# Performance work log

Hardware: AMD Instinct MI355X
Metric: run time of the kernel (lower is better)

Reference implementation:

```python
import jax, jax.numpy as jnp
import numpy as np

N = 100000   # nodes
E = 1600000  # edges
IN = 128     # in_dim
H = 64       # hidden_dim
EPS = 1e-5


def layer_norm(x, g, b):
    mu = x.mean(-1, keepdims=True)
    v = ((x - mu) ** 2).mean(-1, keepdims=True)
    return (x - mu) * jax.lax.rsqrt(v + EPS) * g + b


def gcn_conv(x, W, b, src, dst, dinv):
    # PyG GCNConv: x' = D^{-1/2}(A+I)D^{-1/2} X W + b (degrees include self-loops)
    h = x @ W                                   # [N, H]
    coef = dinv[src] * dinv[dst]                # [E]
    agg = jax.ops.segment_sum(h[src] * coef[:, None], dst, num_segments=N)
    agg = agg + h * (dinv * dinv)[:, None]      # self-loop term
    return agg + b


def setup_inputs() -> dict:
    key = jax.random.key(0)
    ks = jax.random.split(key, 12)
    inp = {
        "x": jax.random.normal(ks[0], (N, IN), jnp.float32),
        "edge_index": jax.random.randint(ks[1], (2, E), 0, N, dtype=jnp.int64
                                         if jax.config.jax_enable_x64 else jnp.int32),
    }
    dims = [(IN, H), (H, H), (H, H)]
    for i, (di, do) in enumerate(dims, start=1):
        inp[f"W{i}"] = jax.random.normal(ks[2 * i], (di, do), jnp.float32) / np.sqrt(di)
        inp[f"b{i}"] = jnp.zeros((do,), jnp.float32)
        inp[f"g{i}"] = jnp.ones((do,), jnp.float32)
        inp[f"be{i}"] = jnp.zeros((do,), jnp.float32)
    inp["Wh"] = jax.random.normal(ks[11], (H, 1), jnp.float32) / np.sqrt(H)
    inp["bh"] = jnp.zeros((1,), jnp.float32)
    return inp


def reference(x, edge_index, W1, b1, g1, be1, W2, b2, g2, be2, W3, b3, g3, be3, Wh, bh):
    src, dst = edge_index[0], edge_index[1]
    deg = jax.ops.segment_sum(jnp.ones((E,), x.dtype), dst, num_segments=N) + 1.0
    dinv = jax.lax.rsqrt(deg)
    for W, b, g, be in ((W1, b1, g1, be1), (W2, b2, g2, be2), (W3, b3, g3, be3)):
        x = gcn_conv(x, W, b, src, dst, dinv)
        x = layer_norm(x, g, be)
        x = jax.nn.gelu(x, approximate=False)  # F.gelu default = exact erf
        # dropout omitted (eval mode / deterministic reference)
    return (x @ Wh + bh).squeeze(-1)  # [N]
```

## Files before the change

### kernel.cpp

```cpp
#include <hip/hip_runtime.h>
#include <math.h>

#define NODES 100000
#define EDGES 1600000
#define SCAN_CHUNK 1024
#define NBUCK 196
#define BCAP2 12288
#define EPB 4096

typedef __attribute__((ext_vector_type(8))) short short8;
typedef __attribute__((ext_vector_type(4))) float floatx4;

__device__ __forceinline__ float half_sum(float x) {
#pragma unroll
  for (int o = 16; o > 0; o >>= 1) x += __shfl_xor(x, o, 64);
  return x;
}

__device__ __forceinline__ short f2bf(float f) {
  union { float f; unsigned u; } v;
  v.f = f;
  unsigned r = 0x7fffu + ((v.u >> 16) & 1u);
  return (short)((v.u + r) >> 16);
}
__device__ __forceinline__ float bf2f(short s) {
  union { unsigned u; float f; } v;
  v.u = ((unsigned)(unsigned short)s) << 16;
  return v.f;
}
__device__ __forceinline__ float bflo(unsigned p) {
  union { unsigned u; float f; } v; v.u = p << 16; return v.f;
}
__device__ __forceinline__ float bfhi(unsigned p) {
  union { unsigned u; float f; } v; v.u = p & 0xffff0000u; return v.f;
}

__global__ __launch_bounds__(256) void k_bin2(const int* __restrict__ src,
                                              const int* __restrict__ dst,
                                              int* __restrict__ bins,
                                              int* __restrict__ gcur) {
  __shared__ int cnt[NBUCK], gbase[NBUCK], lcur[NBUCK];
  int t = threadIdx.x;
  for (int i = t; i < NBUCK; i += 256) cnt[i] = 0;
  __syncthreads();
  int base = blockIdx.x * EPB;
  int s[16], d[16];
#pragma unroll
  for (int j = 0; j < 16; ++j) {
    int e = base + j * 256 + t;
    if (e < EDGES) {
      s[j] = src[e];
      d[j] = dst[e];
      atomicAdd(&cnt[d[j] >> 9], 1);
    } else {
      d[j] = -1;
    }
  }
  __syncthreads();
  for (int i = t; i < NBUCK; i += 256) {
    int c = cnt[i];
    gbase[i] = c ? atomicAdd(&gcur[i], c) : 0;
    lcur[i] = 0;
  }
  __syncthreads();
#pragma unroll
  for (int j = 0; j < 16; ++j) {
    if (d[j] >= 0) {
      int bk = d[j] >> 9;
      int lp = atomicAdd(&lcur[bk], 1);
      int pos = gbase[bk] + lp;
      if (pos < BCAP2) bins[bk * BCAP2 + pos] = s[j] | ((d[j] & 511) << 17);
    }
  }
}

__global__ __launch_bounds__(256) void k_hist(const int* __restrict__ bins,
                                              const int* __restrict__ gcur,
                                              int* __restrict__ deg,
                                              float* __restrict__ dinv) {
  __shared__ int cnt[512];
  int b = blockIdx.x, t = threadIdx.x;
  cnt[t] = 0; cnt[t + 256] = 0;
  __syncthreads();
  int c = gcur[b]; if (c > BCAP2) c = BCAP2;
  const int* bp = &bins[b * BCAP2];
  for (int i = t; i < c; i += 256)
    atomicAdd(&cnt[(bp[i] >> 17) & 511], 1);
  __syncthreads();
#pragma unroll
  for (int k = 0; k < 2; ++k) {
    int n = b * 512 + t + k * 256;
    if (n < NODES) {
      int cc = cnt[t + k * 256];
      deg[n] = cc;
      dinv[n] = rsqrtf((float)cc + 1.0f);
    }
  }
}

__global__ void k_scan1(const int* __restrict__ deg, int* __restrict__ part) {
  __shared__ int sw[4];
  int b = blockIdx.x, t = threadIdx.x;
  int base = b * SCAN_CHUNK;
  int s = 0;
#pragma unroll
  for (int j = 0; j < 4; ++j) {
    int i = base + t * 4 + j;
    if (i < NODES) s += deg[i];
  }
  for (int o = 32; o > 0; o >>= 1) s += __shfl_xor(s, o, 64);
  if ((t & 63) == 0) sw[t >> 6] = s;
  __syncthreads();
  if (t == 0) part[b] = sw[0] + sw[1] + sw[2] + sw[3];
}

__global__ void k_scan2(int* part, int nb) {
  __shared__ int sm[128];
  int t = threadIdx.x;
  int v = (t < nb) ? part[t] : 0;
  sm[t] = v;
  __syncthreads();
  for (int o = 1; o < 128; o <<= 1) {
    int u = (t >= o) ? sm[t - o] : 0;
    __syncthreads();
    sm[t] += u;
    __syncthreads();
  }
  if (t < nb) part[t] = sm[t] - v;
}

__global__ void k_scan3(const int* __restrict__ deg, const int* __restrict__ part,
                        int* __restrict__ rowptr) {
  __shared__ int wtot[4];
  int b = blockIdx.x, t = threadIdx.x;
  int lane = t & 63, wid = t >> 6;
  int base = b * SCAN_CHUNK;
  int d[4];
  int s = 0;
#pragma unroll
  for (int j = 0; j < 4; ++j) {
    int i = base + t * 4 + j;
    d[j] = (i < NODES) ? deg[i] : 0;
    s += d[j];
  }
  int inc = s;
#pragma unroll
  for (int o = 1; o < 64; o <<= 1) {
    int u = __shfl_up(inc, o, 64);
    if (lane >= o) inc += u;
  }
  if (lane == 63) wtot[wid] = inc;
  __syncthreads();
  int wpre = 0;
  for (int w = 0; w < wid; ++w) wpre += wtot[w];
  int off = part[b] + wpre + inc - s;
#pragma unroll
  for (int j = 0; j < 4; ++j) {
    int i = base + t * 4 + j;
    if (i < NODES) { rowptr[i] = off; off += d[j]; }
  }
  if (b == 0 && t == 0) rowptr[NODES] = EDGES;
}

__global__ __launch_bounds__(256) void k_fillb(const int* __restrict__ bins,
                                               const int* __restrict__ gcur,
                                               const int* __restrict__ rowptr,
                                               int* __restrict__ csr) {
  __shared__ int cur[512];
  int b = blockIdx.x, t = threadIdx.x;
#pragma unroll
  for (int k = 0; k < 2; ++k) {
    int n = b * 512 + t + k * 256;
    cur[t + k * 256] = (n < NODES) ? rowptr[n] : 0;
  }
  __syncthreads();
  int c = gcur[b]; if (c > BCAP2) c = BCAP2;
  const int* bp = &bins[b * BCAP2];
  for (int i = t; i < c; i += 256) {
    int pk = bp[i];
    int p = atomicAdd(&cur[(pk >> 17) & 511], 1);
    csr[p] = pk & 0x1FFFF;
  }
}

template <int K>
__global__ __launch_bounds__(256) void k_gemm_f32(const float* __restrict__ x,
                                                  const float* __restrict__ W,
                                                  const float* __restrict__ dinv,
                                                  short* __restrict__ hs) {
  constexpr int KP = K + 8;
  __shared__ short wt[64 * KP];
  for (int idx = threadIdx.x; idx < K * 64; idx += 256) {
    int k = idx >> 6, n = idx & 63;
    wt[n * KP + k] = f2bf(W[idx]);
  }
  __syncthreads();
  int wid = threadIdx.x >> 6, lane = threadIdx.x & 63;
  int tile = blockIdx.x * 4 + wid;
  if (tile * 16 >= NODES) return;
  int m = lane & 15, q = lane >> 4;

  short8 bfr[4][K / 32];
#pragma unroll
  for (int ct = 0; ct < 4; ++ct)
#pragma unroll
    for (int ks = 0; ks < K / 32; ++ks)
      bfr[ct][ks] = *reinterpret_cast<const short8*>(&wt[(ct * 16 + m) * KP + ks * 32 + q * 8]);

  floatx4 acc[4];
#pragma unroll
  for (int ct = 0; ct < 4; ++ct) acc[ct] = {0.f, 0.f, 0.f, 0.f};
  int r0 = tile * 16;
#pragma unroll
  for (int ks = 0; ks < K / 32; ++ks) {
    const float* xp = &x[(size_t)(r0 + m) * K + ks * 32 + q * 8];
    floatx4 a0 = *reinterpret_cast<const floatx4*>(xp);
    floatx4 a1 = *reinterpret_cast<const floatx4*>(xp + 4);
    short8 af;
#pragma unroll
    for (int j = 0; j < 4; ++j) { af[j] = f2bf(a0[j]); af[4 + j] = f2bf(a1[j]); }
#pragma unroll
    for (int ct = 0; ct < 4; ++ct)
      acc[ct] = __builtin_amdgcn_mfma_f32_16x16x32_bf16(af, bfr[ct][ks], acc[ct], 0, 0, 0);
  }
  float dv[4];
#pragma unroll
  for (int r = 0; r < 4; ++r) dv[r] = dinv[r0 + q * 4 + r];
#pragma unroll
  for (int ct = 0; ct < 4; ++ct)
#pragma unroll
    for (int r = 0; r < 4; ++r) {
      int row = r0 + q * 4 + r, col = ct * 16 + m;
      hs[row * 64 + col] = f2bf(acc[ct][r] * dv[r]);
    }
}

__global__ __launch_bounds__(256) void k_gemm_bf(const short* __restrict__ x,
                                                 const float* __restrict__ W,
                                                 const float* __restrict__ dinv,
                                                 short* __restrict__ hs) {
  constexpr int K = 64, KP = K + 8;
  __shared__ short wt[64 * KP];
  for (int idx = threadIdx.x; idx < K * 64; idx += 256) {
    int k = idx >> 6, n = idx & 63;
    wt[n * KP + k] = f2bf(W[idx]);
  }
  __syncthreads();
  int wid = threadIdx.x >> 6, lane = threadIdx.x & 63;
  int tile = blockIdx.x * 4 + wid;
  if (tile * 16 >= NODES) return;
  int m = lane & 15, q = lane >> 4;

  short8 bfr[4][2];
#pragma unroll
  for (int ct = 0; ct < 4; ++ct)
#pragma unroll
    for (int ks = 0; ks < 2; ++ks)
      bfr[ct][ks] = *reinterpret_cast<const short8*>(&wt[(ct * 16 + m) * KP + ks * 32 + q * 8]);

  floatx4 acc[4];
#pragma unroll
  for (int ct = 0; ct < 4; ++ct) acc[ct] = {0.f, 0.f, 0.f, 0.f};
  int r0 = tile * 16;
#pragma unroll
  for (int ks = 0; ks < 2; ++ks) {
    short8 af = *reinterpret_cast<const short8*>(&x[(size_t)(r0 + m) * K + ks * 32 + q * 8]);
#pragma unroll
    for (int ct = 0; ct < 4; ++ct)
      acc[ct] = __builtin_amdgcn_mfma_f32_16x16x32_bf16(af, bfr[ct][ks], acc[ct], 0, 0, 0);
  }
  float dv[4];
#pragma unroll
  for (int r = 0; r < 4; ++r) dv[r] = dinv[r0 + q * 4 + r];
#pragma unroll
  for (int ct = 0; ct < 4; ++ct)
#pragma unroll
    for (int r = 0; r < 4; ++r) {
      int row = r0 + q * 4 + r, col = ct * 16 + m;
      hs[row * 64 + col] = f2bf(acc[ct][r] * dv[r]);
    }
}

template <int FINAL>
__global__ __launch_bounds__(256) void k_agg(const short* __restrict__ hs,
                                             const float* __restrict__ dinv,
                                             const int* __restrict__ rowptr,
                                             const int* __restrict__ csr,
                                             const float* __restrict__ bias,
                                             const float* __restrict__ gam,
                                             const float* __restrict__ bet,
                                             const float* __restrict__ Wh,
                                             const float* __restrict__ bh,
                                             void* __restrict__ out) {
  const unsigned* hsu = (const unsigned*)hs;
  int wid = threadIdx.x >> 6, lane = threadIdx.x & 63;
  int ll = lane & 31, hb = lane & 32;
  int n = blockIdx.x * 8 + wid * 2 + (hb >> 5);
  int e0 = rowptr[n], e1 = rowptr[n + 1];
  float dn = dinv[n];
  unsigned sv = hsu[(size_t)n * 32 + ll];
  float a0 = bflo(sv), a1 = bfhi(sv);
  for (int base = e0; base < e1; base += 8) {
    int cnt = e1 - base;
    if (cnt > 8) cnt = 8;
    int a = base + (ll < cnt ? ll : 0);
    int sidx = csr[a];
    int s[8];
#pragma unroll
    for (int j = 0; j < 8; ++j) s[j] = __shfl(sidx, hb + j, 64);
    unsigned v[8];
#pragma unroll
    for (int j = 0; j < 8; ++j) v[j] = hsu[(size_t)s[j] * 32 + ll];
#pragma unroll
    for (int j = 0; j < 8; ++j) {
      if (j < cnt) { a0 += bflo(v[j]); a1 += bfhi(v[j]); }
    }
  }
  float2 bi = ((const float2*)bias)[ll];
  a0 = a0 * dn + bi.x;
  a1 = a1 * dn + bi.y;
  float mu = half_sum(a0 + a1) * (1.0f / 64.0f);
  float d0 = a0 - mu, d1 = a1 - mu;
  float var = half_sum(d0 * d0 + d1 * d1) * (1.0f / 64.0f);
  float rs = rsqrtf(var + 1e-5f);
  float2 gm = ((const float2*)gam)[ll];
  float2 bt = ((const float2*)bet)[ll];
  float v0 = d0 * rs * gm.x + bt.x;
  float v1 = d1 * rs * gm.y + bt.y;
  float u0 = 0.5f * v0 * (1.0f + erff(v0 * 0.70710678118654752f));
  float u1 = 0.5f * v1 * (1.0f + erff(v1 * 0.70710678118654752f));
  if (FINAL) {
    float2 wh = ((const float2*)Wh)[ll];
    float p = half_sum(u0 * wh.x + u1 * wh.y);
    if (ll == 0) ((float*)out)[n] = p + bh[0];
  } else {
    unsigned pk = (unsigned)(unsigned short)f2bf(u0) |
                  ((unsigned)(unsigned short)f2bf(u1) << 16);
    ((unsigned*)out)[(size_t)n * 32 + ll] = pk;
  }
}

extern "C" void kernel_launch(void* const* d_in, const int* in_sizes, int n_in,
                              void* d_out, int out_size, void* d_ws, size_t ws_size,
                              hipStream_t stream) {
  const float* x  = (const float*)d_in[0];
  const int* ei   = (const int*)d_in[1];
  const float* W1 = (const float*)d_in[2];
  const float* b1 = (const float*)d_in[3];
  const float* g1 = (const float*)d_in[4];
  const float* be1= (const float*)d_in[5];
  const float* W2 = (const float*)d_in[6];
  const float* b2 = (const float*)d_in[7];
  const float* g2 = (const float*)d_in[8];
  const float* be2= (const float*)d_in[9];
  const float* W3 = (const float*)d_in[10];
  const float* b3 = (const float*)d_in[11];
  const float* g3 = (const float*)d_in[12];
  const float* be3= (const float*)d_in[13];
  const float* Wh = (const float*)d_in[14];
  const float* bh = (const float*)d_in[15];
  const int* srcp = ei;
  const int* dstp = ei + EDGES;

  char* ws = (char*)d_ws;
  size_t off = 0;
  auto take = [&](size_t bytes) {
    char* p = ws + off;
    off = (off + bytes + 255) & ~(size_t)255;
    return p;
  };
  int* deg    = (int*)take((size_t)NODES * 4);
  float* dinv = (float*)take((size_t)NODES * 4);
  int* rowptr = (int*)take((size_t)(NODES + 1) * 4);
  int* part   = (int*)take(512);
  int* csr    = (int*)take((size_t)EDGES * 4);
  short* hs   = (short*)take((size_t)NODES * 64 * 2);
  short* xb   = (short*)take((size_t)NODES * 64 * 2);
  int* bins   = (int*)hs;
  int* gcur   = (int*)xb;

  (void)hipMemsetAsync(gcur, 0, (size_t)NBUCK * 4, stream);
  k_bin2<<<(EDGES + EPB - 1) / EPB, 256, 0, stream>>>(srcp, dstp, bins, gcur);
  k_hist<<<NBUCK, 256, 0, stream>>>(bins, gcur, deg, dinv);
  int nb = (NODES + SCAN_CHUNK - 1) / SCAN_CHUNK;
  k_scan1<<<nb, 256, 0, stream>>>(deg, part);
  k_scan2<<<1, 128, 0, stream>>>(part, nb);
  k_scan3<<<nb, 256, 0, stream>>>(deg, part, rowptr);
  k_fillb<<<NBUCK, 256, 0, stream>>>(bins, gcur, rowptr, csr);

  int gemm_grid = (NODES / 16 + 3) / 4;
  k_gemm_f32<128><<<gemm_grid, 256, 0, stream>>>(x, W1, dinv, hs);
  k_agg<0><<<NODES / 8, 256, 0, stream>>>(hs, dinv, rowptr, csr, b1, g1, be1, nullptr, nullptr, xb);
  k_gemm_bf<<<gemm_grid, 256, 0, stream>>>(xb, W2, dinv, hs);
  k_agg<0><<<NODES / 8, 256, 0, stream>>>(hs, dinv, rowptr, csr, b2, g2, be2, nullptr, nullptr, xb);
  k_gemm_bf<<<gemm_grid, 256, 0, stream>>>(xb, W3, dinv, hs);
  k_agg<1><<<NODES / 8, 256, 0, stream>>>(hs, dinv, rowptr, csr, b3, g3, be3, Wh, bh, d_out);
}
```

Measured before the change: 316.9 us.

## Aggregate with 8 lanes per node using 16-byte vector gathers

Restructures the aggregation kernel so each node is handled by 8 lanes, each loading 16 bytes (8 bf16 features), instead of 32 lanes loading 4 bytes each. Each wave now processes 8 nodes, which cuts per-edge instruction count and shuffle overhead and issues wider gather loads. A fast path skips the per-edge predicate when a full batch of 8 edges is present. The trade-off is more registers per lane (8 outstanding 16-byte loads) and fewer lanes per row.

```diff
diff --git a/kernel.cpp b/kernel.cpp
--- a/kernel.cpp
+++ b/kernel.cpp
@@ -10,10 +10,11 @@
 
 typedef __attribute__((ext_vector_type(8))) short short8;
 typedef __attribute__((ext_vector_type(4))) float floatx4;
-
-__device__ __forceinline__ float half_sum(float x) {
-#pragma unroll
-  for (int o = 16; o > 0; o >>= 1) x += __shfl_xor(x, o, 64);
+typedef __attribute__((ext_vector_type(4))) unsigned uv4;
+
+__device__ __forceinline__ float gsum8(float x) {
+#pragma unroll
+  for (int o = 4; o > 0; o >>= 1) x += __shfl_xor(x, o, 64);
   return x;
 }
 
@@ -22,11 +23,6 @@
   v.f = f;
   unsigned r = 0x7fffu + ((v.u >> 16) & 1u);
   return (short)((v.u + r) >> 16);
-}
-__device__ __forceinline__ float bf2f(short s) {
-  union { unsigned u; float f; } v;
-  v.u = ((unsigned)(unsigned short)s) << 16;
-  return v.f;
 }
 __device__ __forceinline__ float bflo(unsigned p) {
   union { unsigned u; float f; } v; v.u = p << 16; return v.f;
@@ -292,51 +288,83 @@
                                              const float* __restrict__ Wh,
                                              const float* __restrict__ bh,
                                              void* __restrict__ out) {
-  const unsigned* hsu = (const unsigned*)hs;
-  int wid = threadIdx.x >> 6, lane = threadIdx.x & 63;
-  int ll = lane & 31, hb = lane & 32;
-  int n = blockIdx.x * 8 + wid * 2 + (hb >> 5);
+  const uv4* hsv = (const uv4*)hs;
+  int lane = threadIdx.x & 63, wid = threadIdx.x >> 6;
+  int g = lane >> 3, q = lane & 7;
+  int n = blockIdx.x * 32 + wid * 8 + g;
   int e0 = rowptr[n], e1 = rowptr[n + 1];
   float dn = dinv[n];
-  unsigned sv = hsu[(size_t)n * 32 + ll];
-  float a0 = bflo(sv), a1 = bfhi(sv);
+  uv4 sv = hsv[(size_t)n * 8 + q];
+  float acc[8];
+#pragma unroll
+  for (int w = 0; w < 4; ++w) { acc[2 * w] = bflo(sv[w]); acc[2 * w + 1] = bfhi(sv[w]); }
+
+  int srcb = lane & 0x38;
   for (int base = e0; base < e1; base += 8) {
     int cnt = e1 - base;
     if (cnt > 8) cnt = 8;
-    int a = base + (ll < cnt ? ll : 0);
+    int a = base + (q < cnt ? q : 0);
     int sidx = csr[a];
     int s[8];
 #pragma unroll
-    for (int j = 0; j < 8; ++j) s[j] = __shfl(sidx, hb + j, 64);
-    unsigned v[8];
-#pragma unroll
-    for (int j = 0; j < 8; ++j) v[j] = hsu[(size_t)s[j] * 32 + ll];
-#pragma unroll
-    for (int j = 0; j < 8; ++j) {
-      if (j < cnt) { a0 += bflo(v[j]); a1 += bfhi(v[j]); }
-    }
-  }
-  float2 bi = ((const float2*)bias)[ll];
-  a0 = a0 * dn + bi.x;
-  a1 = a1 * dn + bi.y;
-  float mu = half_sum(a0 + a1) * (1.0f / 64.0f);
-  float d0 = a0 - mu, d1 = a1 - mu;
-  float var = half_sum(d0 * d0 + d1 * d1) * (1.0f / 64.0f);
-  float rs = rsqrtf(var + 1e-5f);
-  float2 gm = ((const float2*)gam)[ll];
-  float2 bt = ((const float2*)bet)[ll];
-  float v0 = d0 * rs * gm.x + bt.x;
-  float v1 = d1 * rs * gm.y + bt.y;
-  float u0 = 0.5f * v0 * (1.0f + erff(v0 * 0.70710678118654752f));
-  float u1 = 0.5f * v1 * (1.0f + erff(v1 * 0.70710678118654752f));
+    for (int j = 0; j < 8; ++j) s[j] = __shfl(sidx, srcb | j, 64);
+    uv4 v[8];
+#pragma unroll
+    for (int j = 0; j < 8; ++j) v[j] = hsv[(size_t)s[j] * 8 + q];
+    if (cnt == 8) {
+#pragma unroll
+      for (int j = 0; j < 8; ++j)
+#pragma unroll
+        for (int w = 0; w < 4; ++w) { acc[2 * w] += bflo(v[j][w]); acc[2 * w + 1] += bfhi(v[j][w]); }
+    } else {
+#pragma unroll
+      for (int j = 0; j < 8; ++j)
+        if (j < cnt)
+#pragma unroll
+          for (int w = 0; w < 4; ++w) { acc[2 * w] += bflo(v[j][w]); acc[2 * w + 1] += bfhi(v[j][w]); }
+    }
+  }
+
+  const floatx4* bi4 = (const floatx4*)bias;
+  floatx4 b0 = bi4[q * 2], b1 = bi4[q * 2 + 1];
+#pragma unroll
+  for (int f = 0; f < 4; ++f) { acc[f] = acc[f] * dn + b0[f]; acc[f + 4] = acc[f + 4] * dn + b1[f]; }
+
+  float lsum = 0.f;
+#pragma unroll
+  for (int f = 0; f < 8; ++f) lsum += acc[f];
+  float mu = gsum8(lsum) * (1.0f / 64.0f);
+  float d[8], lvar = 0.f;
+#pragma unroll
+  for (int f = 0; f < 8; ++f) { d[f] = acc[f] - mu; lvar += d[f] * d[f]; }
+  float rs = rsqrtf(gsum8(lvar) * (1.0f / 64.0f) + 1e-5f);
+  const floatx4* gm4 = (const floatx4*)gam;
+  const floatx4* bt4 = (const floatx4*)bet;
+  floatx4 g0 = gm4[q * 2], g1 = gm4[q * 2 + 1];
+  floatx4 t0 = bt4[q * 2], t1 = bt4[q * 2 + 1];
+  float u[8];
+#pragma unroll
+  for (int f = 0; f < 8; ++f) {
+    float gv = (f < 4) ? g0[f] : g1[f - 4];
+    float tv = (f < 4) ? t0[f] : t1[f - 4];
+    float vv = d[f] * rs * gv + tv;
+    u[f] = 0.5f * vv * (1.0f + erff(vv * 0.70710678118654752f));
+  }
   if (FINAL) {
-    float2 wh = ((const float2*)Wh)[ll];
-    float p = half_sum(u0 * wh.x + u1 * wh.y);
-    if (ll == 0) ((float*)out)[n] = p + bh[0];
+    const floatx4* wh4 = (const floatx4*)Wh;
+    floatx4 w0 = wh4[q * 2], w1 = wh4[q * 2 + 1];
+    float lp = 0.f;
+#pragma unroll
+    for (int f = 0; f < 4; ++f) lp += u[f] * w0[f] + u[f + 4] * w1[f];
+    float p = gsum8(lp);
+    if (q == 0) ((float*)out)[n] = p + bh[0];
   } else {
-    unsigned pk = (unsigned)(unsigned short)f2bf(u0) |
-                  ((unsigned)(unsigned short)f2bf(u1) << 16);
-    ((unsigned*)out)[(size_t)n * 32 + ll] = pk;
+    uv4 pk;
+#pragma unroll
+    for (int w = 0; w < 4; ++w)
+      pk[w] = (unsigned)(unsigned short)f2bf(u[2 * w]) |
+              ((unsigned)(unsigned short)f2bf(u[2 * w + 1]) << 16);
+    ((uv4*)out)[(size_t)n * 8 + q] = pk;
   }
 }
 
@@ -390,9 +418,9 @@
 
   int gemm_grid = (NODES / 16 + 3) / 4;
   k_gemm_f32<128><<<gemm_grid, 256, 0, stream>>>(x, W1, dinv, hs);
-  k_agg<0><<<NODES / 8, 256, 0, stream>>>(hs, dinv, rowptr, csr, b1, g1, be1, nullptr, nullptr, xb);
+  k_agg<0><<<NODES / 32, 256, 0, stream>>>(hs, dinv, rowptr, csr, b1, g1, be1, nullptr, nullptr, xb);
   k_gemm_bf<<<gemm_grid, 256, 0, stream>>>(xb, W2, dinv, hs);
-  k_agg<0><<<NODES / 8, 256, 0, stream>>>(hs, dinv, rowptr, csr, b2, g2, be2, nullptr, nullptr, xb);
+  k_agg<0><<<NODES / 32, 256, 0, stream>>>(hs, dinv, rowptr, csr, b2, g2, be2, nullptr, nullptr, xb);
   k_gemm_bf<<<gemm_grid, 256, 0, stream>>>(xb, W3, dinv, hs);
-  k_agg<1><<<NODES / 8, 256, 0, stream>>>(hs, dinv, rowptr, csr, b3, g3, be3, Wh, bh, d_out);
-}
+  k_agg<1><<<NODES / 32, 256, 0, stream>>>(hs, dinv, rowptr, csr, b3, g3, be3, Wh, bh, d_out);
+}
```

Measured after the change: 298.6 us. 5.8% less time.
